# Optimization experiments

Measured on AMD Instinct MI355X. Metric: run time of the kernel, lower is better.

Reference implementation:

```python
import jax, jax.numpy as jnp
import numpy as np

L_K = 3  # conv kernel width l


def _conv1d_shared(x, w):
    """x: [B, C, L], w: [l]. out[b,c,i] = sum_j x[b,c,i+j]*w[j] (kernel shared over channels).
    Matches torch Conv1d class: bmm of [B,C,l] slices with [l,1] weight."""
    l = w.shape[0]
    Lo = x.shape[-1] - l + 1
    out = jnp.zeros(x.shape[:2] + (Lo,), dtype=x.dtype)
    for j in range(l):  # small fixed loop over kernel taps
        out = out + x[:, :, j:j + Lo] * w[j]
    return out


def setup_inputs() -> dict:
    key = jax.random.key(0)
    k1, k2, k3, k4, k5 = jax.random.split(key, 5)
    B, S, D, H = 8192, 30, 512, 1024
    return {
        "emb": jax.random.normal(k1, (B, S, D), dtype=jnp.float32),
        "w_long": jax.random.uniform(k2, (L_K,), dtype=jnp.float32),
        "w_mid": jax.random.uniform(k3, (L_K,), dtype=jnp.float32),
        "W1": jax.random.normal(k4, (H, 3 * D), dtype=jnp.float32) * 0.02,
        "W2": jax.random.normal(k5, (1, H), dtype=jnp.float32) * 0.02,
    }


def reference(emb, w_long, w_mid, W1, W2):
    # emb: [B, 30, D]
    x = jnp.swapaxes(emb, 1, 2)                 # [B, D, 30]
    vl = _conv1d_shared(x, w_long).max(axis=-1)  # conv len 28, maxpool(28) -> [B, D]
    xm = x[:, :, -7:]                            # last 7 steps
    vm = _conv1d_shared(xm, w_mid).max(axis=-1)  # conv len 5, maxpool(5) -> [B, D]
    vs = emb[:, -1, :]                           # [B, D]
    feature = jnp.concatenate([vl, vm, vs], axis=1)  # [B, 3D]
    hidden = jnp.tanh(feature @ W1.T)                # [B, H]
    out = hidden @ W2.T                              # [B, 1]
    return out[:, 0]
```

## Files before the change

kernel.cpp:

```cpp
#include <hip/hip_runtime.h>


#define B_   8192
#define S_   30
#define D_   512
#define H_   1024
#define K_   1536

typedef float nf4 __attribute__((ext_vector_type(4)));

__device__ inline unsigned short f2bf(float f) {
    unsigned int u = __float_as_uint(f);
    u += 0x7FFFu + ((u >> 16) & 1u);
    return (unsigned short)(u >> 16);
}

__device__ inline nf4 fmax4(nf4 a, nf4 b) {
    nf4 r;
    r.x = fmaxf(a.x, b.x); r.y = fmaxf(a.y, b.y);
    r.z = fmaxf(a.z, b.z); r.w = fmaxf(a.w, b.w);
    return r;
}

__device__ inline void store_bf4(unsigned short* p, nf4 v) {
    ushort4 o;
    o.x = f2bf(v.x); o.y = f2bf(v.y); o.z = f2bf(v.z); o.w = f2bf(v.w);
    *(ushort4*)p = o;
}

__device__ inline nf4 ntload4(const float* p) {
    return __builtin_nontemporal_load((const nf4*)p);
}

__global__ __launch_bounds__(256) void feat_kernel(
    const float* __restrict__ emb, const float* __restrict__ wl,
    const float* __restrict__ wm, unsigned short* __restrict__ feat)
{
    int gid = blockIdx.x * 256 + threadIdx.x;
    int b   = gid >> 7;
    int c4  = (gid & 127) << 2;

    const float* base = emb + (size_t)b * (S_ * D_) + c4;
    const float l0 = wl[0], l1 = wl[1], l2 = wl[2];
    const float m0 = wm[0], m1 = wm[1], m2 = wm[2];

    nf4 e0 = ntload4(base + 0 * D_);
    nf4 e1 = ntload4(base + 1 * D_);
    nf4 vl = {-3.4e38f, -3.4e38f, -3.4e38f, -3.4e38f};
    nf4 vm = vl;

    #pragma unroll 4
    for (int i = 0; i < 28; ++i) {
        nf4 e2 = ntload4(base + (i + 2) * D_);
        nf4 cv = e0 * l0 + e1 * l1 + e2 * l2;
        vl = fmax4(vl, cv);
        if (i >= 23) {
            nf4 cm = e0 * m0 + e1 * m1 + e2 * m2;
            vm = fmax4(vm, cm);
        }
        e0 = e1; e1 = e2;
    }
    unsigned short* frow = feat + (size_t)b * K_;
    store_bf4(frow + c4,            vl);
    store_bf4(frow + D_ + c4,       vm);
    store_bf4(frow + 2 * D_ + c4,   e1);
}

__global__ __launch_bounds__(256) void w1conv_kernel(
    const float* __restrict__ W1, unsigned short* __restrict__ w1b)
{
    int gid = blockIdx.x * 256 + threadIdx.x;
    nf4 v = ((const nf4*)W1)[gid];
    ushort4 o;
    o.x = f2bf(v.x); o.y = f2bf(v.y); o.z = f2bf(v.z); o.w = f2bf(v.w);
    ((ushort4*)w1b)[gid] = o;
}


typedef __bf16 bf16x8 __attribute__((ext_vector_type(8)));
typedef float  f32x4  __attribute__((ext_vector_type(4)));

#define GL2LDS(gp, lp) __builtin_amdgcn_global_load_lds( \
    (const __attribute__((address_space(1))) void*)(gp), \
    (__attribute__((address_space(3))) void*)(lp), 16, 0, 0)

__global__ __launch_bounds__(256) void gemm_kernel(
    const unsigned short* __restrict__ A,
    const unsigned short* __restrict__ Bm,
    const float* __restrict__ W2,
    float* __restrict__ out)
{
    __shared__ unsigned short As[128 * 32];
    __shared__ unsigned short Bs[128 * 32];

    const int tid  = threadIdx.x;
    const int bm   = (blockIdx.x >> 3) * 128;
    const int bn   = (blockIdx.x & 7) * 128;
    const int wave = tid >> 6;
    const int lane = tid & 63;
    const int wm   = wave >> 1;
    const int wn   = wave & 1;
    const int lrow = lane & 15;
    const int quad = lane >> 4;

    f32x4 acc[4][4] = {};

    const int srow = tid >> 2;
    const int skof = (tid & 3) * 8;
    const unsigned short* a_src0 = A  + (size_t)(bm + srow) * K_ + skof;
    const unsigned short* a_src1 = a_src0 + (size_t)64 * K_;
    const unsigned short* b_src0 = Bm + (size_t)(bn + srow) * K_ + skof;
    const unsigned short* b_src1 = b_src0 + (size_t)64 * K_;
    unsigned short* a_dst0 = &As[(size_t)tid * 8];
    unsigned short* a_dst1 = &As[(size_t)(tid + 256) * 8];
    unsigned short* b_dst0 = &Bs[(size_t)tid * 8];
    unsigned short* b_dst1 = &Bs[(size_t)(tid + 256) * 8];

    for (int kt = 0; kt < K_ / 32; ++kt) {
        const int ko = kt * 32;
        GL2LDS(a_src0 + ko, a_dst0);
        GL2LDS(a_src1 + ko, a_dst1);
        GL2LDS(b_src0 + ko, b_dst0);
        GL2LDS(b_src1 + ko, b_dst1);
        __syncthreads();

        bf16x8 af[4], bf[4];
        #pragma unroll
        for (int mi = 0; mi < 4; ++mi)
            af[mi] = *(const bf16x8*)&As[(wm * 64 + mi * 16 + lrow) * 32 + quad * 8];
        #pragma unroll
        for (int ni = 0; ni < 4; ++ni)
            bf[ni] = *(const bf16x8*)&Bs[(wn * 64 + ni * 16 + lrow) * 32 + quad * 8];

        #pragma unroll
        for (int mi = 0; mi < 4; ++mi)
            #pragma unroll
            for (int ni = 0; ni < 4; ++ni)
                acc[mi][ni] = __builtin_amdgcn_mfma_f32_16x16x32_bf16(
                    af[mi], bf[ni], acc[mi][ni], 0, 0, 0);

        __syncthreads();
    }

    float w2v[4];
    #pragma unroll
    for (int ni = 0; ni < 4; ++ni)
        w2v[ni] = W2[bn + wn * 64 + ni * 16 + lrow];

    #pragma unroll
    for (int mi = 0; mi < 4; ++mi) {
        #pragma unroll
        for (int r = 0; r < 4; ++r) {
            float s = 0.f;
            #pragma unroll
            for (int ni = 0; ni < 4; ++ni)
                s += tanhf(acc[mi][ni][r]) * w2v[ni];
            #pragma unroll
            for (int off = 1; off < 16; off <<= 1)
                s += __shfl_xor(s, off, 64);
            if (lrow == 0)
                atomicAdd(&out[bm + wm * 64 + mi * 16 + quad * 4 + r], s);
        }
    }
}

extern "C" void kernel_launch(void* const* d_in, const int* in_sizes, int n_in,
                              void* d_out, int out_size, void* d_ws, size_t ws_size,
                              hipStream_t stream) {
    const float* emb = (const float*)d_in[0];
    const float* wl  = (const float*)d_in[1];
    const float* wm  = (const float*)d_in[2];
    const float* W1  = (const float*)d_in[3];
    const float* W2  = (const float*)d_in[4];
    float* out = (float*)d_out;

    unsigned short* feat = (unsigned short*)d_ws;
    unsigned short* w1b  = feat + (size_t)B_ * K_;

    (void)hipMemsetAsync(out, 0, sizeof(float) * B_, stream);

    hipLaunchKernelGGL(feat_kernel, dim3(B_ * (D_ / 4) / 256), dim3(256), 0, stream,
                       emb, wl, wm, feat);
    hipLaunchKernelGGL(w1conv_kernel, dim3(H_ * K_ / 4 / 256), dim3(256), 0, stream,
                       W1, w1b);
    hipLaunchKernelGGL(gemm_kernel, dim3((B_ / 128) * (H_ / 128)), dim3(256), 0, stream,
                       feat, w1b, W2, out);
}
```

Measured before the change: 679.5 us.

## Double GEMM K-tile to 64 with XOR-swizzled LDS and fast tanh

The GEMM K-step grows from 32 to 64, which halves the number of barrier pairs per tile. Each thread now issues four global-to-LDS loads per operand, and LDS columns are XOR-swizzled by row to avoid bank conflicts on the 128-byte row stride. The epilogue swaps tanhf for a clamped exp-based tanh to cut transcendental cost. This doubles LDS use per block, which may affect occupancy, and the approximate tanh adds slight numerical error.

```diff
diff --git a/kernel.cpp b/kernel.cpp
--- a/kernel.cpp
+++ b/kernel.cpp
@@ -30,6 +30,12 @@
 
 __device__ inline nf4 ntload4(const float* p) {
     return __builtin_nontemporal_load((const nf4*)p);
+}
+
+__device__ inline float fast_tanh(float x) {
+    float cx = fminf(fmaxf(x, -15.f), 15.f);
+    float e = __expf(2.f * cx);
+    return (e - 1.f) / (e + 1.f);
 }
 
 __global__ __launch_bounds__(256) void feat_kernel(
@@ -90,54 +96,59 @@
     const float* __restrict__ W2,
     float* __restrict__ out)
 {
-    __shared__ unsigned short As[128 * 32];
-    __shared__ unsigned short Bs[128 * 32];
+    __shared__ unsigned short As[128 * 64];
+    __shared__ unsigned short Bs[128 * 64];
 
     const int tid  = threadIdx.x;
     const int bm   = (blockIdx.x >> 3) * 128;
     const int bn   = (blockIdx.x & 7) * 128;
-    const int wave = tid >> 6;
     const int lane = tid & 63;
-    const int wm   = wave >> 1;
-    const int wn   = wave & 1;
+    const int wm   = (tid >> 6) >> 1;
+    const int wn   = (tid >> 6) & 1;
     const int lrow = lane & 15;
     const int quad = lane >> 4;
 
     f32x4 acc[4][4] = {};
 
-    const int srow = tid >> 2;
-    const int skof = (tid & 3) * 8;
-    const unsigned short* a_src0 = A  + (size_t)(bm + srow) * K_ + skof;
-    const unsigned short* a_src1 = a_src0 + (size_t)64 * K_;
-    const unsigned short* b_src0 = Bm + (size_t)(bn + srow) * K_ + skof;
-    const unsigned short* b_src1 = b_src0 + (size_t)64 * K_;
-    unsigned short* a_dst0 = &As[(size_t)tid * 8];
-    unsigned short* a_dst1 = &As[(size_t)(tid + 256) * 8];
-    unsigned short* b_dst0 = &Bs[(size_t)tid * 8];
-    unsigned short* b_dst1 = &Bs[(size_t)(tid + 256) * 8];
+    int s_row[4], s_jof[4];
+    #pragma unroll
+    for (int jj = 0; jj < 4; ++jj) {
+        int q = tid + jj * 256;
+        s_row[jj] = q >> 3;
+        s_jof[jj] = (((q & 7) ^ (s_row[jj] & 7)) * 8);
+    }
 
-    for (int kt = 0; kt < K_ / 32; ++kt) {
-        const int ko = kt * 32;
-        GL2LDS(a_src0 + ko, a_dst0);
-        GL2LDS(a_src1 + ko, a_dst1);
-        GL2LDS(b_src0 + ko, b_dst0);
-        GL2LDS(b_src1 + ko, b_dst1);
+    for (int kt = 0; kt < K_ / 64; ++kt) {
+        const int ko = kt * 64;
+        #pragma unroll
+        for (int jj = 0; jj < 4; ++jj) {
+            int q = tid + jj * 256;
+            GL2LDS(A  + (size_t)(bm + s_row[jj]) * K_ + ko + s_jof[jj], &As[q * 8]);
+            GL2LDS(Bm + (size_t)(bn + s_row[jj]) * K_ + ko + s_jof[jj], &Bs[q * 8]);
+        }
         __syncthreads();
 
-        bf16x8 af[4], bf[4];
         #pragma unroll
-        for (int mi = 0; mi < 4; ++mi)
-            af[mi] = *(const bf16x8*)&As[(wm * 64 + mi * 16 + lrow) * 32 + quad * 8];
-        #pragma unroll
-        for (int ni = 0; ni < 4; ++ni)
-            bf[ni] = *(const bf16x8*)&Bs[(wn * 64 + ni * 16 + lrow) * 32 + quad * 8];
-
-        #pragma unroll
-        for (int mi = 0; mi < 4; ++mi)
+        for (int kk = 0; kk < 2; ++kk) {
+            bf16x8 af[4], bf[4];
+            const int j = kk * 4 + quad;
             #pragma unroll
-            for (int ni = 0; ni < 4; ++ni)
-                acc[mi][ni] = __builtin_amdgcn_mfma_f32_16x16x32_bf16(
-                    af[mi], bf[ni], acc[mi][ni], 0, 0, 0);
+            for (int mi = 0; mi < 4; ++mi) {
+                int r = wm * 64 + mi * 16 + lrow;
+                af[mi] = *(const bf16x8*)&As[r * 64 + ((j ^ (r & 7)) * 8)];
+            }
+            #pragma unroll
+            for (int ni = 0; ni < 4; ++ni) {
+                int r = wn * 64 + ni * 16 + lrow;
+                bf[ni] = *(const bf16x8*)&Bs[r * 64 + ((j ^ (r & 7)) * 8)];
+            }
+            #pragma unroll
+            for (int mi = 0; mi < 4; ++mi)
+                #pragma unroll
+                for (int ni = 0; ni < 4; ++ni)
+                    acc[mi][ni] = __builtin_amdgcn_mfma_f32_16x16x32_bf16(
+                        af[mi], bf[ni], acc[mi][ni], 0, 0, 0);
+        }
 
         __syncthreads();
     }
@@ -154,7 +165,7 @@
             float s = 0.f;
             #pragma unroll
             for (int ni = 0; ni < 4; ++ni)
-                s += tanhf(acc[mi][ni][r]) * w2v[ni];
+                s += fast_tanh(acc[mi][ni][r]) * w2v[ni];
             #pragma unroll
             for (int off = 1; off < 16; off <<= 1)
                 s += __shfl_xor(s, off, 64);
```

Measured after the change: 670.8 us. Within noise of the previous version (-1.3%).
